# Performance work log

Measured on AMD Instinct MI355X. Metric: run time of the kernel, lower is better.

## Reference

```python
import jax, jax.numpy as jnp
import numpy as np

HUMAN_EXHALATION_FLOW = 0.0052  # ENV_CONFIG.HUMAN_EXHALATION_FLOW
TIME_STEP = 1.0                 # ENV_CONFIG.TIME_STEP
N_NODES = 100_000
N_EDGES = 3_200_000
IN_DIM, OUT_DIM, K = 4, 1, 3
T_HIST = 16


def setup_inputs() -> dict:
    key = jax.random.key(0)
    k1, k2, k3, k4, k5 = jax.random.split(key, 5)
    # columns at [:, -1, :]: 0=concentration, 1=people, 2=size (size divides -> keep away from 0)
    origin_data = jax.random.uniform(k1, (N_NODES, T_HIST, 3), jnp.float32, 0.5, 1.5)
    # raw flow field: conv with kernel K (VALID) maps [E+K-1, K, IN_DIM] -> [E, 1, OUT_DIM]
    flow = jax.random.normal(k2, (N_EDGES + K - 1, K, IN_DIM), jnp.float32)
    edge_index = jax.random.randint(k3, (2, N_EDGES), 0, N_NODES, jnp.int32)
    conv_w = jax.random.normal(k4, (OUT_DIM, IN_DIM, K, K), jnp.float32) * 0.1
    conv_b = jax.random.normal(k5, (OUT_DIM,), jnp.float32) * 0.1
    return {"origin_data": origin_data, "flow": flow, "conv_w": conv_w,
            "conv_b": conv_b, "edge_index": edge_index}


def _flow_conv(flow, conv_w, conv_b):
    # [H, W, C] -> [1, C, H, W] -> conv -> [H', W', out_dim]
    x = jnp.transpose(flow, (2, 0, 1))[None]
    y = jax.lax.conv_general_dilated(
        x, conv_w, window_strides=(1, 1), padding='VALID',
        dimension_numbers=('NCHW', 'OIHW', 'NCHW'))
    y = y + conv_b[None, :, None, None]
    return jnp.transpose(y[0], (1, 2, 0))  # [E, 1, out_dim]


def reference(origin_data, flow, conv_w, conv_b, edge_index):
    concentration = origin_data[:, -1, 0]  # [N]
    people = origin_data[:, -1, 1]         # [N]
    size = origin_data[:, -1, 2]           # [N]
    n = concentration.shape[0]
    mask = jnp.ones((n,), concentration.dtype).at[-1].set(0.0)

    fc = _flow_conv(flow, conv_w, conv_b)  # [E, 1, 1]
    val = fc[:, 0, 0]                      # [E]

    src, dst = edge_index[0], edge_index[1]
    # original loop uses .item() everywhere -> these terms are detached from autodiff
    c_sg = jax.lax.stop_gradient(concentration)
    s_sg = jax.lax.stop_gradient(size)
    v_sg = jax.lax.stop_gradient(val)
    msg = jnp.where(src != dst, v_sg * c_sg[src], 0.0)  # skip self-loops
    node_new = jnp.zeros((n,), concentration.dtype)
    node_new = node_new.at[src].add(-msg / s_sg[src] * TIME_STEP)
    node_new = node_new.at[dst].add(msg / s_sg[dst] * TIME_STEP)

    exhaled = HUMAN_EXHALATION_FLOW * jax.lax.stop_gradient(people) / s_sg  # .item() loop -> detached
    result = concentration + (node_new + exhaled * TIME_STEP) * mask
    out2 = jnp.concatenate([edge_index.T.astype(val.dtype), fc[:, :, 0]], axis=1)  # [E, 3]
    return result[:, None], out2
```

## Files before the change

kernel.cpp:

```cpp
#include <hip/hip_runtime.h>


#define WSH  14
#define WSZ  16384
#define PBF  32

#define OWSH 13
#define OWSZ 8192
#define OPB  16
#define OFPS 8192.0f
#define OQBIAS (1 << 20)
#define OQCLMP ((1 << 19) - 1)

__global__ __launch_bounds__(256) void prep(
    const float* __restrict__ od,
    float* __restrict__ conc,
    unsigned long long* __restrict__ acc,
    int n_nodes)
{
    int n = blockIdx.x * blockDim.x + threadIdx.x;
    if (n >= n_nodes) return;
    conc[n] = od[(long long)n * 48 + 45];
    if (acc) acc[n] = 0ULL;
}

__global__ __launch_bounds__(256) void edge_conv(
    const float* __restrict__ flow, const int* __restrict__ ei,
    const float* __restrict__ conv_w, const float* __restrict__ conv_b,
    const float* __restrict__ conc,
    float* __restrict__ out2, float* __restrict__ bcv, int n_edges)
{
    __shared__ float w[40];
    __shared__ __align__(16) float4 stg[774];

    const int t = threadIdx.x;
    if (t < 36) {
        int i  = t & 3;
        int kw = (t >> 2) % 3;
        int kh = t / 12;
        w[t] = conv_w[i * 9 + kh * 3 + kw];
    }
    if (t == 36) w[36] = conv_b[0];

    const long long E0 = (long long)blockIdx.x * 256;
    const long long e  = E0 + t;
    const bool live = (e < n_edges);

    int s = 0, d = 0;
    if (live) { s = ei[e]; d = ei[n_edges + e]; }
    float cs = live ? conc[s] : 0.f;

    const long long rows_avail = (long long)n_edges + 2 - E0;
    const int nf4 = (int)(3 * (rows_avail < 258 ? rows_avail : 258));
    const float4* fb = (const float4*)flow + E0 * 3;
    for (int i = t; i < nf4; i += 256) stg[i] = fb[i];
    __syncthreads();

    if (!live) return;

    const float4* fp = &stg[t * 3];
    float acc = w[36];
#pragma unroll
    for (int q = 0; q < 9; ++q) {
        float4 v = fp[q];
        acc = fmaf(v.x, w[q * 4 + 0], acc);
        acc = fmaf(v.y, w[q * 4 + 1], acc);
        acc = fmaf(v.z, w[q * 4 + 2], acc);
        acc = fmaf(v.w, w[q * 4 + 3], acc);
    }

    float* o = out2 + e * 3;
    o[0] = (float)s;
    o[1] = (float)d;
    o[2] = acc;
    bcv[e] = acc * cs;
}

__global__ __launch_bounds__(1024) void accum_f(
    const float* __restrict__ out2,
    const float* __restrict__ bcv,
    float* __restrict__ pA,
    float* __restrict__ pB,
    int n_edges, int n_win, int stride)
{
    __shared__ float tA[WSZ];
    __shared__ float tB[WSZ];

    const int xcd = blockIdx.x & 7;
    const int i   = blockIdx.x >> 3;
    const int j   = i / n_win;
    const int sl  = xcd * (PBF >> 3) + j;
    const int w   = i - j * n_win;

    const int t = threadIdx.x;
    for (int k = t; k < WSZ; k += 1024) { tA[k] = 0.f; tB[k] = 0.f; }
    __syncthreads();

    const long long e0 = (long long)sl * n_edges / PBF;
    const long long e1 = (long long)(sl + 1) * n_edges / PBF;

#define PROC(fs, fd, vv, bb)                                          \
    {                                                                  \
        int s_ = (int)(fs), d_ = (int)(fd);                            \
        if (s_ != d_) {                                                \
            if ((s_ >> WSH) == w) atomicAdd(&tA[s_ & (WSZ - 1)], (vv));\
            if ((d_ >> WSH) == w) atomicAdd(&tB[d_ & (WSZ - 1)], (bb));\
        }                                                              \
    }

    long long e = e0 + t;
    for (; e + 3 * 1024 < e1; e += 4 * 1024) {
        const float* r  = out2 + e * 3;
        const float* bb = bcv + e;
        float fs0 = r[0],    fd0 = r[1],    v0 = r[2];
        float fs1 = r[3072], fd1 = r[3073], v1 = r[3074];
        float fs2 = r[6144], fd2 = r[6145], v2 = r[6146];
        float fs3 = r[9216], fd3 = r[9217], v3 = r[9218];
        float b0 = bb[0], b1 = bb[1024], b2 = bb[2048], b3 = bb[3072];
        PROC(fs0, fd0, v0, b0);
        PROC(fs1, fd1, v1, b1);
        PROC(fs2, fd2, v2, b2);
        PROC(fs3, fd3, v3, b3);
    }
    for (; e < e1; e += 1024) {
        const float* r = out2 + e * 3;
        float fs = r[0], fd = r[1], vv = r[2];
        float bb = bcv[e];
        PROC(fs, fd, vv, bb);
    }
#undef PROC
    __syncthreads();

    float* dA = pA + (long long)sl * stride + ((long long)w << WSH);
    float* dB = pB + (long long)sl * stride + ((long long)w << WSH);
    for (int k = t; k < (WSZ >> 2); k += 1024) {
        ((float4*)dA)[k] = ((const float4*)tA)[k];
        ((float4*)dB)[k] = ((const float4*)tB)[k];
    }
}

__global__ __launch_bounds__(256) void node_final_f(
    const float* __restrict__ od,
    const float* __restrict__ conc,
    const float* __restrict__ pA,
    const float* __restrict__ pB,
    float* __restrict__ out, int n_nodes, int stride)
{
    const int n0 = (blockIdx.x * 256 + threadIdx.x) * 4;
    if (n0 >= n_nodes) return;

    if (n0 + 4 <= n_nodes) {
        float4 a = make_float4(0.f, 0.f, 0.f, 0.f);
        float4 b = make_float4(0.f, 0.f, 0.f, 0.f);
#pragma unroll 8
        for (int sl = 0; sl < PBF; ++sl) {
            float4 va = *(const float4*)(pA + (size_t)sl * stride + n0);
            float4 vb = *(const float4*)(pB + (size_t)sl * stride + n0);
            a.x += va.x; a.y += va.y; a.z += va.z; a.w += va.w;
            b.x += vb.x; b.y += vb.y; b.z += vb.z; b.w += vb.w;
        }
        float4 c4 = *(const float4*)(conc + n0);
        float av[4] = {a.x, a.y, a.z, a.w};
        float bv[4] = {b.x, b.y, b.z, b.w};
        float cv[4] = {c4.x, c4.y, c4.z, c4.w};
        float rv[4];
#pragma unroll
        for (int j = 0; j < 4; ++j) {
            int n = n0 + j;
            long long bi = (long long)n * 48 + 45;
            float p  = od[bi + 1];
            float is = 1.0f / od[bi + 2];
            float r = cv[j];
            if (n != n_nodes - 1)
                r += (bv[j] - av[j] * cv[j]) * is + 0.0052f * p * is;
            rv[j] = r;
        }
        *(float4*)(out + n0) = make_float4(rv[0], rv[1], rv[2], rv[3]);
    } else {
        for (int n = n0; n < n_nodes; ++n) {
            float a = 0.f, b = 0.f;
#pragma unroll 8
            for (int sl = 0; sl < PBF; ++sl) {
                a += pA[(size_t)sl * stride + n];
                b += pB[(size_t)sl * stride + n];
            }
            long long bi = (long long)n * 48 + 45;
            float c  = conc[n];
            float p  = od[bi + 1];
            float is = 1.0f / od[bi + 2];
            float r = c;
            if (n != n_nodes - 1)
                r += (b - a * c) * is + 0.0052f * p * is;
            out[n] = r;
        }
    }
}

__global__ __launch_bounds__(256) void edge_conv_o(
    const float* __restrict__ flow, const int* __restrict__ ei,
    const float* __restrict__ conv_w, const float* __restrict__ conv_b,
    float* __restrict__ out2, int n_edges)
{
    __shared__ float w[40];
    int t = threadIdx.x;
    if (t < 36) {
        int i  = t & 3;
        int kw = (t >> 2) % 3;
        int kh = t / 12;
        w[t] = conv_w[i * 9 + kh * 3 + kw];
    }
    if (t == 36) w[36] = conv_b[0];
    __syncthreads();

    int e = blockIdx.x * blockDim.x + t;
    if (e >= n_edges) return;

    const float4* fp = (const float4*)(flow + (long long)e * 12);
    float acc = w[36];
#pragma unroll
    for (int q = 0; q < 9; ++q) {
        float4 v = fp[q];
        acc = fmaf(v.x, w[q * 4 + 0], acc);
        acc = fmaf(v.y, w[q * 4 + 1], acc);
        acc = fmaf(v.z, w[q * 4 + 2], acc);
        acc = fmaf(v.w, w[q * 4 + 3], acc);
    }

    float* o = out2 + (long long)e * 3;
    o[0] = (float)ei[e];
    o[1] = (float)ei[n_edges + e];
    o[2] = acc;
}

__global__ __launch_bounds__(1024) void accum_o(
    const float* __restrict__ out2,
    const float* __restrict__ conc,
    unsigned long long* __restrict__ acc,
    int n_edges, int n_nodes)
{
    __shared__ float tA[OWSZ];
    __shared__ float tB[OWSZ];

    const int w    = blockIdx.x / OPB;
    const int sl   = blockIdx.x % OPB;
    const int base = w << OWSH;

    for (int i = threadIdx.x; i < OWSZ; i += 1024) { tA[i] = 0.f; tB[i] = 0.f; }
    __syncthreads();

    const long long e0 = (long long)sl * n_edges / OPB;
    const long long e1 = (long long)(sl + 1) * n_edges / OPB;
    for (long long e = e0 + threadIdx.x; e < e1; e += 1024) {
        const float* r = out2 + e * 3;
        float fs = r[0], fd = r[1], v = r[2];
        int s = (int)fs, d = (int)fd;
        if (s == d) continue;
        if ((s >> OWSH) == w) atomicAdd(&tA[s - base], v);
        if ((d >> OWSH) == w) atomicAdd(&tB[d - base], v * conc[s]);
    }
    __syncthreads();

    for (int i = threadIdx.x; i < OWSZ; i += 1024) {
        int n = base + i;
        if (n >= n_nodes) continue;
        float a = tA[i], b = tB[i];
        if (a == 0.f && b == 0.f) continue;
        int qa = __float2int_rn(a * OFPS);
        int qb = __float2int_rn(b * OFPS);
        qa = min(max(qa, -OQCLMP), OQCLMP);
        qb = min(max(qb, -OQCLMP), OQCLMP);
        unsigned long long enc =
            ((unsigned long long)(unsigned)(qa + OQBIAS) << 37) +
            ((unsigned long long)(unsigned)(qb + OQBIAS) << 10) + 1ULL;
        atomicAdd(acc + n, enc);
    }
}

__global__ __launch_bounds__(256) void node_final_o(
    const float* __restrict__ od,
    const float* __restrict__ conc,
    const unsigned long long* __restrict__ acc,
    float* __restrict__ out, int n_nodes)
{
    int n = blockIdx.x * blockDim.x + threadIdx.x;
    if (n >= n_nodes) return;

    unsigned long long t = acc[n];
    long long cnt = (long long)(t & 1023ULL);
    unsigned long long t2 = t >> 10;
    long long sbr = (long long)(t2 & ((1ULL << 27) - 1));
    long long sar = (long long)(t2 >> 27);
    float a = (float)(sar - cnt * OQBIAS) * (1.0f / OFPS);
    float b = (float)(sbr - cnt * OQBIAS) * (1.0f / OFPS);

    long long bi = (long long)n * 48 + 45;
    float c  = conc[n];
    float p  = od[bi + 1];
    float is = 1.0f / od[bi + 2];

    float r = c;
    if (n != n_nodes - 1)
        r += (b - a * c) * is + 0.0052f * p * is;
    out[n] = r;
}

extern "C" void kernel_launch(void* const* d_in, const int* in_sizes, int n_in,
                              void* d_out, int out_size, void* d_ws, size_t ws_size,
                              hipStream_t stream) {
    const float* od   = (const float*)d_in[0];
    const float* flow = (const float*)d_in[1];
    const float* cw   = (const float*)d_in[2];
    const float* cb   = (const float*)d_in[3];
    const int*   ei   = (const int*)d_in[4];

    const int n_nodes = in_sizes[0] / 48;
    const int n_edges = in_sizes[4] / 2;

    float* out_res = (float*)d_out;
    float* out2    = out_res + n_nodes;

    dim3 blk(256);
    dim3 grid_nodes((n_nodes + 255) / 256);

    const int n_win  = (n_nodes + WSZ - 1) >> WSH;
    const int stride = n_win << WSH;
    size_t off = 0;
    size_t o_conc = off; off += (((size_t)n_nodes * 4) + 255) & ~255ULL;
    size_t o_bc   = off; off += (((size_t)n_edges * 4) + 255) & ~255ULL;
    size_t o_pA   = off; off += (((size_t)PBF * stride * 4) + 255) & ~255ULL;
    size_t o_pB   = off; off += (((size_t)PBF * stride * 4) + 255) & ~255ULL;
    const bool full = (ws_size >= off);

    float* conc = (float*)((char*)d_ws + o_conc);

    if (full) {
        float* bcv = (float*)((char*)d_ws + o_bc);
        float* pA  = (float*)((char*)d_ws + o_pA);
        float* pB  = (float*)((char*)d_ws + o_pB);

        dim3 grid_ec((n_edges + 255) / 256);
        dim3 grid_nf(((n_nodes + 3) / 4 + 255) / 256);

        prep<<<grid_nodes, blk, 0, stream>>>(od, conc, nullptr, n_nodes);
        edge_conv<<<grid_ec, blk, 0, stream>>>(flow, ei, cw, cb, conc,
                                               out2, bcv, n_edges);
        accum_f<<<dim3(n_win * PBF), dim3(1024), 0, stream>>>(
            out2, bcv, pA, pB, n_edges, n_win, stride);
        node_final_f<<<grid_nf, blk, 0, stream>>>(od, conc, pA, pB,
                                                  out_res, n_nodes, stride);
    } else {
        unsigned long long* acc =
            (unsigned long long*)((char*)d_ws + (((size_t)n_nodes * 4 + 7) / 8 * 8));
        const int n_win_o = (n_nodes + OWSZ - 1) >> OWSH;
        dim3 grid_edges((n_edges + 255) / 256);

        prep<<<grid_nodes, blk, 0, stream>>>(od, conc, acc, n_nodes);
        edge_conv_o<<<grid_edges, blk, 0, stream>>>(flow, ei, cw, cb, out2, n_edges);
        accum_o<<<dim3(n_win_o * OPB), dim3(1024), 0, stream>>>(
            out2, conc, acc, n_edges, n_nodes);
        node_final_o<<<grid_nodes, blk, 0, stream>>>(od, conc, acc,
                                                     out_res, n_nodes);
    }
}
```

Baseline: 327.0 us.

## Split accumulation into separate src/dst record streams and accumulate kernels

The edge kernel now writes two packed 8-byte records per edge, (src key, value) and (dst key, value*conc). A self-loop is encoded as an out-of-range key so it never matches a window. The accumulate kernel is split along blockIdx.y into independent A and B passes, each with a single shared-memory table. That halves LDS per block, allowing more resident blocks, and removes the float-to-int index conversion and the self-loop branch. The cost is extra workspace and edge-kernel writes (16 B per edge instead of 4 B). Each accumulate block also rereads its slice of records per window, so total record traffic changes from 16 B to 16 B per edge per window but is now split across twice as many blocks.

After: 333.5 us. Within noise of the previous version (+2.0%).

```diff
diff --git a/kernel.cpp b/kernel.cpp
--- a/kernel.cpp
+++ b/kernel.cpp
@@ -28,7 +28,8 @@
     const float* __restrict__ flow, const int* __restrict__ ei,
     const float* __restrict__ conv_w, const float* __restrict__ conv_b,
     const float* __restrict__ conc,
-    float* __restrict__ out2, float* __restrict__ bcv, int n_edges)
+    float* __restrict__ out2,
+    uint2* __restrict__ recA, uint2* __restrict__ recB, int n_edges)
 {
     __shared__ float w[40];
     __shared__ __align__(16) float4 stg[774];
@@ -73,18 +74,21 @@
     o[0] = (float)s;
     o[1] = (float)d;
     o[2] = acc;
-    bcv[e] = acc * cs;
-}
-
-__global__ __launch_bounds__(1024) void accum_f(
-    const float* __restrict__ out2,
-    const float* __restrict__ bcv,
-    float* __restrict__ pA,
-    float* __restrict__ pB,
+
+    unsigned sk = (s == d) ? 0xFFFFFFFFu : (unsigned)s;
+    unsigned dk = (s == d) ? 0xFFFFFFFFu : (unsigned)d;
+    uint2 ra; ra.x = sk; ra.y = __float_as_uint(acc);
+    uint2 rb; rb.x = dk; rb.y = __float_as_uint(acc * cs);
+    recA[e] = ra;
+    recB[e] = rb;
+}
+
+__global__ __launch_bounds__(1024) void accum_ab(
+    const uint2* __restrict__ recA, const uint2* __restrict__ recB,
+    float* __restrict__ pA, float* __restrict__ pB,
     int n_edges, int n_win, int stride)
 {
-    __shared__ float tA[WSZ];
-    __shared__ float tB[WSZ];
+    __shared__ float tbl[WSZ];
 
     const int xcd = blockIdx.x & 7;
     const int i   = blockIdx.x >> 3;
@@ -92,51 +96,38 @@
     const int sl  = xcd * (PBF >> 3) + j;
     const int w   = i - j * n_win;
 
+    const uint2* rec = blockIdx.y ? recB : recA;
+    float*       par = blockIdx.y ? pB  : pA;
+
     const int t = threadIdx.x;
-    for (int k = t; k < WSZ; k += 1024) { tA[k] = 0.f; tB[k] = 0.f; }
+    for (int k = t; k < WSZ; k += 1024) tbl[k] = 0.f;
     __syncthreads();
 
     const long long e0 = (long long)sl * n_edges / PBF;
     const long long e1 = (long long)(sl + 1) * n_edges / PBF;
 
-#define PROC(fs, fd, vv, bb)                                          \
-    {                                                                  \
-        int s_ = (int)(fs), d_ = (int)(fd);                            \
-        if (s_ != d_) {                                                \
-            if ((s_ >> WSH) == w) atomicAdd(&tA[s_ & (WSZ - 1)], (vv));\
-            if ((d_ >> WSH) == w) atomicAdd(&tB[d_ & (WSZ - 1)], (bb));\
-        }                                                              \
-    }
+#define PROC(r)                                                        \
+    if ((int)((r).x >> WSH) == w)                                      \
+        atomicAdd(&tbl[(r).x & (WSZ - 1)], __uint_as_float((r).y));
 
     long long e = e0 + t;
     for (; e + 3 * 1024 < e1; e += 4 * 1024) {
-        const float* r  = out2 + e * 3;
-        const float* bb = bcv + e;
-        float fs0 = r[0],    fd0 = r[1],    v0 = r[2];
-        float fs1 = r[3072], fd1 = r[3073], v1 = r[3074];
-        float fs2 = r[6144], fd2 = r[6145], v2 = r[6146];
-        float fs3 = r[9216], fd3 = r[9217], v3 = r[9218];
-        float b0 = bb[0], b1 = bb[1024], b2 = bb[2048], b3 = bb[3072];
-        PROC(fs0, fd0, v0, b0);
-        PROC(fs1, fd1, v1, b1);
-        PROC(fs2, fd2, v2, b2);
-        PROC(fs3, fd3, v3, b3);
+        uint2 r0 = rec[e];
+        uint2 r1 = rec[e + 1024];
+        uint2 r2 = rec[e + 2048];
+        uint2 r3 = rec[e + 3072];
+        PROC(r0); PROC(r1); PROC(r2); PROC(r3);
     }
     for (; e < e1; e += 1024) {
-        const float* r = out2 + e * 3;
-        float fs = r[0], fd = r[1], vv = r[2];
-        float bb = bcv[e];
-        PROC(fs, fd, vv, bb);
+        uint2 r = rec[e];
+        PROC(r);
     }
 #undef PROC
     __syncthreads();
 
-    float* dA = pA + (long long)sl * stride + ((long long)w << WSH);
-    float* dB = pB + (long long)sl * stride + ((long long)w << WSH);
-    for (int k = t; k < (WSZ >> 2); k += 1024) {
-        ((float4*)dA)[k] = ((const float4*)tA)[k];
-        ((float4*)dB)[k] = ((const float4*)tB)[k];
-    }
+    float* dst = par + (long long)sl * stride + ((long long)w << WSH);
+    for (int k = t; k < (WSZ >> 2); k += 1024)
+        ((float4*)dst)[k] = ((const float4*)tbl)[k];
 }
 
 __global__ __launch_bounds__(256) void node_final_f(
@@ -326,7 +317,8 @@
     const int stride = n_win << WSH;
     size_t off = 0;
     size_t o_conc = off; off += (((size_t)n_nodes * 4) + 255) & ~255ULL;
-    size_t o_bc   = off; off += (((size_t)n_edges * 4) + 255) & ~255ULL;
+    size_t o_rA   = off; off += (((size_t)n_edges * 8) + 255) & ~255ULL;
+    size_t o_rB   = off; off += (((size_t)n_edges * 8) + 255) & ~255ULL;
     size_t o_pA   = off; off += (((size_t)PBF * stride * 4) + 255) & ~255ULL;
     size_t o_pB   = off; off += (((size_t)PBF * stride * 4) + 255) & ~255ULL;
     const bool full = (ws_size >= off);
@@ -334,18 +326,19 @@
     float* conc = (float*)((char*)d_ws + o_conc);
 
     if (full) {
-        float* bcv = (float*)((char*)d_ws + o_bc);
-        float* pA  = (float*)((char*)d_ws + o_pA);
-        float* pB  = (float*)((char*)d_ws + o_pB);
+        uint2* recA = (uint2*)((char*)d_ws + o_rA);
+        uint2* recB = (uint2*)((char*)d_ws + o_rB);
+        float* pA   = (float*)((char*)d_ws + o_pA);
+        float* pB   = (float*)((char*)d_ws + o_pB);
 
         dim3 grid_ec((n_edges + 255) / 256);
         dim3 grid_nf(((n_nodes + 3) / 4 + 255) / 256);
 
         prep<<<grid_nodes, blk, 0, stream>>>(od, conc, nullptr, n_nodes);
         edge_conv<<<grid_ec, blk, 0, stream>>>(flow, ei, cw, cb, conc,
-                                               out2, bcv, n_edges);
-        accum_f<<<dim3(n_win * PBF), dim3(1024), 0, stream>>>(
-            out2, bcv, pA, pB, n_edges, n_win, stride);
+                                               out2, recA, recB, n_edges);
+        accum_ab<<<dim3(n_win * PBF, 2), dim3(1024), 0, stream>>>(
+            recA, recB, pA, pB, n_edges, n_win, stride);
         node_final_f<<<grid_nf, blk, 0, stream>>>(od, conc, pA, pB,
                                                   out_res, n_nodes, stride);
     } else {
```
